# Performance work log

Measured on AMD Instinct MI355X. Metric: run time of the kernel, lower is better.

The kernel has to match this reference:

```python
import jax, jax.numpy as jnp
import numpy as np

B, C, H, Wd = 4, 2048, 64, 64
HID = 256


def setup_inputs() -> dict:
    key = jax.random.key(0)
    k1, k2, k3, k4 = jax.random.split(key, 4)
    return {
        "query_features": jax.random.normal(k1, (B, C, H, Wd), dtype=jnp.float32),
        "prompt_features": jax.random.normal(k2, (B, C, H, Wd), dtype=jnp.float32),
        "W": jax.random.normal(k3, (HID, C), dtype=jnp.float32) * (1.0 / np.sqrt(C)),
        "b": jax.random.normal(k4, (HID,), dtype=jnp.float32) * 0.02,
    }


def reference(query_features, prompt_features, W, b):
    # 1x1 conv == channel projection
    Q = jnp.einsum('bchw,oc->bohw', query_features, W) + b[None, :, None, None]
    K = jnp.einsum('bchw,oc->bohw', prompt_features, W) + b[None, :, None, None]
    Bq, Cf, Hq, Wq = prompt_features.shape
    V = prompt_features.reshape(Bq, Cf, Hq * Wq)              # b c p
    # full pairwise score tensor: bijkl -> b i j (k l)
    attn = jnp.einsum('bcij,bckl->bijkl', Q, K).reshape(Bq, Hq, Wq, Hq * Wq)
    attn = jax.nn.softmax(attn, axis=3)
    aligned = jnp.einsum('bijp,bcp->bcij', attn, V)           # b c h w
    return aligned
```

## Files before the change

### kernel.cpp

```cpp
#include <hip/hip_runtime.h>
#include <math.h>


#define BATCH 4
#define CH    2048
#define PP    4096
#define DD    256

typedef __bf16    bf16x8 __attribute__((ext_vector_type(8)));
typedef _Float16  f16x8  __attribute__((ext_vector_type(8)));
typedef _Float16  f16x4  __attribute__((ext_vector_type(4)));
typedef float     f32x4  __attribute__((ext_vector_type(4)));

__device__ __forceinline__ unsigned short f2bf(float f) {
  unsigned int u = __float_as_uint(f);
  unsigned int r = u + 0x7fffu + ((u >> 16) & 1u);
  return (unsigned short)(r >> 16);
}

#define GLL(src, dst) \
  __builtin_amdgcn_global_load_lds( \
      (const __attribute__((address_space(1))) unsigned int*)(uintptr_t)(src), \
      (__attribute__((address_space(3))) unsigned int*)(uintptr_t)(dst), 16, 0, 0)

__global__ __launch_bounds__(256) void prep_w(
    const float* __restrict__ W, _Float16* __restrict__ Wf) {
  int i = blockIdx.x * 256 + threadIdx.x;
  float4 v = ((const float4*)W)[i];
  f16x4 h = {(_Float16)v.x, (_Float16)v.y, (_Float16)v.z, (_Float16)v.w};
  ((f16x4*)Wf)[i] = h;
}

__global__ __launch_bounds__(256) void tsplit8(
    const float* __restrict__ Xq, const float* __restrict__ Xp,
    _Float16* __restrict__ Xt8) {
  const int z = blockIdx.z;
  const float* __restrict__ X =
      ((z & 1) ? Xp : Xq) + (size_t)(z >> 1) * CH * PP;
  _Float16* __restrict__ Xt = Xt8 + (size_t)z * CH * PP;

  __shared__ float Ls[64 * 65];
  const int tid = threadIdx.x;
  const int pBase = blockIdx.x * 64, cBase = blockIdx.y * 64;
#pragma unroll
  for (int i = 0; i < 4; ++i) {
    int e = tid + i * 256;
    int c = e >> 4, p4 = e & 15;
    float4 v = *(const float4*)&X[(size_t)(cBase + c) * PP + pBase + p4 * 4];
    Ls[c * 65 + p4 * 4 + 0] = v.x; Ls[c * 65 + p4 * 4 + 1] = v.y;
    Ls[c * 65 + p4 * 4 + 2] = v.z; Ls[c * 65 + p4 * 4 + 3] = v.w;
  }
  __syncthreads();
#pragma unroll
  for (int j = 0; j < 4; ++j) {
    int p = (tid >> 4) + j * 16;
    int c4 = (tid & 15) * 4;
    f16x4 h = {(_Float16)Ls[(c4 + 0) * 65 + p], (_Float16)Ls[(c4 + 1) * 65 + p],
               (_Float16)Ls[(c4 + 2) * 65 + p], (_Float16)Ls[(c4 + 3) * 65 + p]};
    *(f16x4*)&Xt[(size_t)(pBase + p) * CH + cBase + c4] = h;
  }
}

__global__ __launch_bounds__(256) void proj8(
    const _Float16* __restrict__ Xt8, const _Float16* __restrict__ Wf,
    const float* __restrict__ bias,
    unsigned short* __restrict__ Qh, unsigned short* __restrict__ Ql,
    unsigned short* __restrict__ Kh, unsigned short* __restrict__ Kl) {
  const int z = blockIdx.z;
  const _Float16* __restrict__ Xt = Xt8 + (size_t)z * CH * PP;
  unsigned short* __restrict__ Yh =
      ((z & 1) ? Kh : Qh) + (size_t)(z >> 1) * PP * DD;
  unsigned short* __restrict__ Yl =
      ((z & 1) ? Kl : Ql) + (size_t)(z >> 1) * PP * DD;

  const int pBase = blockIdx.x * 64;
  const int oBase = blockIdx.y * 64;
  const int tid  = threadIdx.x;
  const int wave = tid >> 6;
  const int lane = tid & 63;
  const int wm = wave & 1, wn = wave >> 1;
  const int row16 = lane & 15, quad = lane >> 4, koff = quad * 8;

  __shared__ __align__(16) _Float16 As0[64 * 32], As1[64 * 32];
  __shared__ __align__(16) _Float16 Bs0[64 * 32], Bs1[64 * 32];

  const int sRow = lane >> 2;
  const int sKc  = (lane & 3) * 8;

  f32x4 acc[2][2];
#pragma unroll
  for (int i = 0; i < 2; ++i)
#pragma unroll
    for (int j = 0; j < 2; ++j) acc[i][j] = (f32x4){0.f, 0.f, 0.f, 0.f};

  for (int c0 = 0; c0 < CH; c0 += 64) {
    const int row = wave * 16 + sRow;
    GLL(&Xt[(size_t)(pBase + row) * CH + c0 + sKc],      &As0[(wave * 16) * 32]);
    GLL(&Xt[(size_t)(pBase + row) * CH + c0 + 32 + sKc], &As1[(wave * 16) * 32]);
    GLL(&Wf[(size_t)(oBase + row) * CH + c0 + sKc],      &Bs0[(wave * 16) * 32]);
    GLL(&Wf[(size_t)(oBase + row) * CH + c0 + 32 + sKc], &Bs1[(wave * 16) * 32]);
    __syncthreads();
#pragma unroll
    for (int s = 0; s < 2; ++s) {
      const _Float16* Ap = s ? As1 : As0;
      const _Float16* Bp = s ? Bs1 : Bs0;
      f16x8 af[2], bf[2];
#pragma unroll
      for (int i = 0; i < 2; ++i)
        af[i] = *(const f16x8*)&Ap[(wm * 32 + i * 16 + row16) * 32 + koff];
#pragma unroll
      for (int j = 0; j < 2; ++j)
        bf[j] = *(const f16x8*)&Bp[(wn * 32 + j * 16 + row16) * 32 + koff];
#pragma unroll
      for (int i = 0; i < 2; ++i)
#pragma unroll
        for (int j = 0; j < 2; ++j)
          acc[i][j] = __builtin_amdgcn_mfma_f32_16x16x32_f16(
              af[i], bf[j], acc[i][j], 0, 0, 0);
    }
    __syncthreads();
  }

#pragma unroll
  for (int i = 0; i < 2; ++i)
#pragma unroll
    for (int j = 0; j < 2; ++j) {
      const int ocol = oBase + wn * 32 + j * 16 + row16;
      const float bv = bias[ocol];
#pragma unroll
      for (int r = 0; r < 4; ++r) {
        const int prow = pBase + wm * 32 + i * 16 + quad * 4 + r;
        float y = acc[i][j][r] + bv;
        unsigned short h = f2bf(y);
        float hf = __uint_as_float((unsigned int)h << 16);
        unsigned short l = f2bf(y - hf);
        Yh[(size_t)prow * DD + ocol] = h;
        Yl[(size_t)prow * DD + ocol] = l;
      }
    }
}

__global__ __launch_bounds__(256) void scores8(
    const unsigned short* __restrict__ Qh_, const unsigned short* __restrict__ Ql_,
    const unsigned short* __restrict__ Kh_, const unsigned short* __restrict__ Kl_,
    float* __restrict__ S_) {
  const size_t z = blockIdx.z;
  const unsigned short* __restrict__ Qh = Qh_ + z * (size_t)PP * DD;
  const unsigned short* __restrict__ Ql = Ql_ + z * (size_t)PP * DD;
  const unsigned short* __restrict__ Kh = Kh_ + z * (size_t)PP * DD;
  const unsigned short* __restrict__ Kl = Kl_ + z * (size_t)PP * DD;
  float* __restrict__ S = S_ + z * (size_t)PP * PP;

  const int kBase = blockIdx.x * 128;
  const int pBase = blockIdx.y * 128;
  const int tid  = threadIdx.x;
  const int wave = tid >> 6;
  const int lane = tid & 63;
  const int wm = wave & 1, wn = wave >> 1;
  const int row16 = lane & 15, quad = lane >> 4, koff = quad * 8;

  __shared__ __align__(16) unsigned short Ah[128 * 32], Al[128 * 32];
  __shared__ __align__(16) unsigned short Bh[128 * 32], Bl[128 * 32];

  const int sRow = lane >> 2;
  const int sKc  = (lane & 3) * 8;

  f32x4 acc[4][4];
#pragma unroll
  for (int i = 0; i < 4; ++i)
#pragma unroll
    for (int j = 0; j < 4; ++j) acc[i][j] = (f32x4){0.f, 0.f, 0.f, 0.f};

  for (int d0 = 0; d0 < DD; d0 += 32) {
#pragma unroll
    for (int t = 0; t < 2; ++t) {
      const int rg = wave * 32 + t * 16;
      const int row = rg + sRow;
      GLL(&Qh[(size_t)(pBase + row) * DD + d0 + sKc], &Ah[rg * 32]);
      GLL(&Ql[(size_t)(pBase + row) * DD + d0 + sKc], &Al[rg * 32]);
      GLL(&Kh[(size_t)(kBase + row) * DD + d0 + sKc], &Bh[rg * 32]);
      GLL(&Kl[(size_t)(kBase + row) * DD + d0 + sKc], &Bl[rg * 32]);
    }
    __syncthreads();
    bf16x8 ah[4], al[4], bh[4], bl[4];
#pragma unroll
    for (int i = 0; i < 4; ++i) {
      ah[i] = *(const bf16x8*)&Ah[(wm * 64 + i * 16 + row16) * 32 + koff];
      al[i] = *(const bf16x8*)&Al[(wm * 64 + i * 16 + row16) * 32 + koff];
    }
#pragma unroll
    for (int j = 0; j < 4; ++j) {
      bh[j] = *(const bf16x8*)&Bh[(wn * 64 + j * 16 + row16) * 32 + koff];
      bl[j] = *(const bf16x8*)&Bl[(wn * 64 + j * 16 + row16) * 32 + koff];
    }
#pragma unroll
    for (int i = 0; i < 4; ++i)
#pragma unroll
      for (int j = 0; j < 4; ++j) {
        acc[i][j] = __builtin_amdgcn_mfma_f32_16x16x32_bf16(ah[i], bh[j], acc[i][j], 0, 0, 0);
        acc[i][j] = __builtin_amdgcn_mfma_f32_16x16x32_bf16(ah[i], bl[j], acc[i][j], 0, 0, 0);
        acc[i][j] = __builtin_amdgcn_mfma_f32_16x16x32_bf16(al[i], bh[j], acc[i][j], 0, 0, 0);
      }
    __syncthreads();
  }

#pragma unroll
  for (int i = 0; i < 4; ++i)
#pragma unroll
    for (int j = 0; j < 4; ++j) {
      const int kcol = kBase + wn * 64 + j * 16 + row16;
#pragma unroll
      for (int r = 0; r < 4; ++r) {
        const int prow = pBase + wm * 64 + i * 16 + quad * 4 + r;
        S[(size_t)prow * PP + kcol] = acc[i][j][r];
      }
    }
}

__global__ __launch_bounds__(256) void softmax8(float* __restrict__ S_) {
  float* __restrict__ Sb = S_ + (size_t)blockIdx.y * PP * PP;
  unsigned short* __restrict__ Ab = (unsigned short*)Sb;
  const size_t p = blockIdx.x;
  float* row = Sb + p * PP;
  const int tid = threadIdx.x;
  float4 v[4];
#pragma unroll
  for (int i = 0; i < 4; ++i)
    v[i] = *(const float4*)&row[(i * 256 + tid) * 4];
  float m = -1e30f;
#pragma unroll
  for (int i = 0; i < 4; ++i)
    m = fmaxf(m, fmaxf(fmaxf(v[i].x, v[i].y), fmaxf(v[i].z, v[i].w)));
#pragma unroll
  for (int off = 32; off > 0; off >>= 1)
    m = fmaxf(m, __shfl_xor(m, off));
  __shared__ float red[4];
  const int lane = tid & 63, wv = tid >> 6;
  if (lane == 0) red[wv] = m;
  __syncthreads();
  m = fmaxf(fmaxf(red[0], red[1]), fmaxf(red[2], red[3]));
  __syncthreads();
  float s = 0.f;
#pragma unroll
  for (int i = 0; i < 4; ++i) {
    v[i].x = __expf(v[i].x - m);
    v[i].y = __expf(v[i].y - m);
    v[i].z = __expf(v[i].z - m);
    v[i].w = __expf(v[i].w - m);
    s += v[i].x + v[i].y + v[i].z + v[i].w;
  }
#pragma unroll
  for (int off = 32; off > 0; off >>= 1)
    s += __shfl_xor(s, off);
  if (lane == 0) red[wv] = s;
  __syncthreads();
  s = red[0] + red[1] + red[2] + red[3];
  const float inv = 1.f / s;
  unsigned short* orow = Ab + p * 8192;
#pragma unroll
  for (int i = 0; i < 4; ++i) {
    ushort4 o;
    o.x = f2bf(v[i].x * inv); o.y = f2bf(v[i].y * inv);
    o.z = f2bf(v[i].z * inv); o.w = f2bf(v[i].w * inv);
    *(ushort4*)&orow[(i * 256 + tid) * 4] = o;
  }
}

__global__ __launch_bounds__(256) void cvt_bf16(
    const float* __restrict__ X, unsigned short* __restrict__ Y, int n4) {
  int i = blockIdx.x * blockDim.x + threadIdx.x;
  if (i < n4) {
    float4 v = ((const float4*)X)[i];
    ushort4 o;
    o.x = f2bf(v.x); o.y = f2bf(v.y); o.z = f2bf(v.z); o.w = f2bf(v.w);
    ((ushort4*)Y)[i] = o;
  }
}


#define AOFF(d, h) ((d) * 32768 + (h) * 16384)
#define BOFF(d, h) (65536 + (d) * 32768 + (h) * 16384)

#define PH_READ_A(d, mh) do {                                                  \
  _Pragma("unroll")                                                            \
  for (int m_ = 0; m_ < 4; ++m_) {                                             \
    const int ro_ = AOFF(d, wm) + ((mh) * 64 + m_ * 16 + row16) * 128;         \
    aR[m_][0] = *(const bf16x8*)(Lds + ro_ + cx0);                             \
    aR[m_][1] = *(const bf16x8*)(Lds + ro_ + cx1);                             \
  } } while (0)

#define PH_READ_B(d, nh, breg) do {                                            \
  _Pragma("unroll")                                                            \
  for (int n_ = 0; n_ < 2; ++n_) {                                             \
    const int ro_ = BOFF(d, wnh) + (wnl * 64 + (nh) * 32 + n_ * 16 + row16) * 128; \
    breg[n_][0] = *(const bf16x8*)(Lds + ro_ + cx0);                           \
    breg[n_][1] = *(const bf16x8*)(Lds + ro_ + cx1);                           \
  } } while (0)

#define PH_MFMA(mh, nh, breg) do {                                             \
  __builtin_amdgcn_s_setprio(1);                                               \
  _Pragma("unroll")                                                            \
  for (int m_ = 0; m_ < 4; ++m_)                                               \
  _Pragma("unroll")                                                            \
  for (int n_ = 0; n_ < 2; ++n_) {                                             \
    f32x4 a_ = acc[(mh) * 4 + m_][(nh) * 2 + n_];                              \
    a_ = __builtin_amdgcn_mfma_f32_16x16x32_bf16(aR[m_][0], breg[n_][0], a_, 0, 0, 0); \
    a_ = __builtin_amdgcn_mfma_f32_16x16x32_bf16(aR[m_][1], breg[n_][1], a_, 0, 0, 0); \
    acc[(mh) * 4 + m_][(nh) * 2 + n_] = a_;                                    \
  }                                                                            \
  __builtin_amdgcn_s_setprio(0); } while (0)

#define BAR_MID() do {                                                         \
  __builtin_amdgcn_sched_barrier(0);                                           \
  __builtin_amdgcn_s_barrier();                                                \
  asm volatile("s_waitcnt lgkmcnt(0)" ::: "memory");                           \
  __builtin_amdgcn_sched_barrier(0); } while (0)

#define BAR_END() __builtin_amdgcn_s_barrier()

__global__ __launch_bounds__(512, 2) void out8(
    const unsigned short* __restrict__ V_,
    const unsigned short* __restrict__ A_,
    float* __restrict__ O_) {
  const size_t z = blockIdx.z;
  const unsigned short* __restrict__ Vb = V_ + z * (size_t)CH * PP;
  const unsigned short* __restrict__ Ab = A_ + z * (size_t)PP * 8192;
  float* __restrict__ Ob = O_ + z * (size_t)CH * PP;

  const int pBase = blockIdx.x * 256;
  const int cBase = blockIdx.y * 256;
  const int tid = threadIdx.x;
  const int wave = tid >> 6, lane = tid & 63;
  const int wm = wave >> 2;
  const int wn = wave & 3;
  const int wnh = wn >> 1, wnl = wn & 1;
  const int row16 = lane & 15, quad = lane >> 4;

  __shared__ __align__(16) char Lds[131072];

  const int swz = (row16 & 7) << 4;
  const int cx0 = ((quad) << 4) ^ swz;
  const int cx1 = ((4 + quad) << 4) ^ swz;

  const int stRow0 = (wave * 2 + 0) * 8 + (lane >> 3);
  const int stRow1 = (wave * 2 + 1) * 8 + (lane >> 3);
  const int stCol  = (((lane & 7) ^ (lane >> 3)) << 4);
  char* ldsSt0 = Lds + (wave * 2 + 0) * 1024;
  char* ldsSt1 = Lds + (wave * 2 + 1) * 1024;

  const size_t VLDG = (size_t)PP * 2;
  const size_t ALDG = (size_t)8192 * 2;

  auto STG = [&](int ldsOff, const void* gbase, size_t ldgB, int rowBase, int gkB) {
    const char* g0 = (const char*)gbase + (size_t)(rowBase + stRow0) * ldgB + gkB + stCol;
    const char* g1 = (const char*)gbase + (size_t)(rowBase + stRow1) * ldgB + gkB + stCol;
    GLL(g0, ldsSt0 + ldsOff);
    GLL(g1, ldsSt1 + ldsOff);
  };

  f32x4 acc[8][4];
#pragma unroll
  for (int i = 0; i < 8; ++i)
#pragma unroll
    for (int j = 0; j < 4; ++j) acc[i][j] = (f32x4){0.f, 0.f, 0.f, 0.f};

  bf16x8 aR[4][2], bLo[2][2], bHi[2][2];

  STG(BOFF(0, 0), Ab, ALDG, pBase + 0,   0);
  STG(BOFF(0, 1), Ab, ALDG, pBase + 128, 0);
  STG(AOFF(0, 0), Vb, VLDG, cBase + 0,   0);
  STG(AOFF(0, 1), Vb, VLDG, cBase + 128, 0);
  STG(BOFF(1, 0), Ab, ALDG, pBase + 0,   128);
  STG(BOFF(1, 1), Ab, ALDG, pBase + 128, 128);
  asm volatile("s_waitcnt vmcnt(4)" ::: "memory");
  __builtin_amdgcn_s_barrier();

#pragma unroll 1
  for (int i = 0; i < 31; ++i) {
    const int t = 2 * i;
    const int gk1 = (t + 1) * 128, gk2 = (t + 2) * 128, gk3 = (t + 3) * 128;
    PH_READ_A(0, 0); PH_READ_B(0, 0, bLo);
    STG(AOFF(1, 0), Vb, VLDG, cBase + 0, gk1);
    BAR_MID(); PH_MFMA(0, 0, bLo); BAR_END();
    PH_READ_B(0, 1, bHi);
    STG(AOFF(1, 1), Vb, VLDG, cBase + 128, gk1);
    BAR_MID(); PH_MFMA(0, 1, bHi); BAR_END();
    PH_READ_A(0, 1);
    STG(BOFF(0, 0), Ab, ALDG, pBase + 0, gk2);
    BAR_MID(); PH_MFMA(1, 0, bLo); BAR_END();
    STG(BOFF(0, 1), Ab, ALDG, pBase + 128, gk2);
    BAR_MID(); PH_MFMA(1, 1, bHi);
    asm volatile("s_waitcnt vmcnt(4)" ::: "memory");
    BAR_END();
    PH_READ_A(1, 0); PH_READ_B(1, 0, bLo);
    STG(AOFF(0, 0), Vb, VLDG, cBase + 0, gk2);
    BAR_MID(); PH_MFMA(0, 0, bLo); BAR_END();
    PH_READ_B(1, 1, bHi);
    STG(AOFF(0, 1), Vb, VLDG, cBase + 128, gk2);
    BAR_MID(); PH_MFMA(0, 1, bHi); BAR_END();
    PH_READ_A(1, 1);
    STG(BOFF(1, 0), Ab, ALDG, pBase + 0, gk3);
    BAR_MID(); PH_MFMA(1, 0, bLo); BAR_END();
    STG(BOFF(1, 1), Ab, ALDG, pBase + 128, gk3);
    BAR_MID(); PH_MFMA(1, 1, bHi);
    asm volatile("s_waitcnt vmcnt(4)" ::: "memory");
    BAR_END();
  }

  {
    const int gk1 = 63 * 128;
    PH_READ_A(0, 0); PH_READ_B(0, 0, bLo);
    STG(AOFF(1, 0), Vb, VLDG, cBase + 0, gk1);
    BAR_MID(); PH_MFMA(0, 0, bLo); BAR_END();
    PH_READ_B(0, 1, bHi);
    STG(AOFF(1, 1), Vb, VLDG, cBase + 128, gk1);
    BAR_MID(); PH_MFMA(0, 1, bHi); BAR_END();
    PH_READ_A(0, 1);
    BAR_MID(); PH_MFMA(1, 0, bLo); BAR_END();
    BAR_MID(); PH_MFMA(1, 1, bHi);
    asm volatile("s_waitcnt vmcnt(0)" ::: "memory");
    BAR_END();
    PH_READ_A(1, 0); PH_READ_B(1, 0, bLo);
    BAR_MID(); PH_MFMA(0, 0, bLo); BAR_END();
    PH_READ_B(1, 1, bHi);
    BAR_MID(); PH_MFMA(0, 1, bHi); BAR_END();
    PH_READ_A(1, 1);
    BAR_MID(); PH_MFMA(1, 0, bLo); BAR_END();
    BAR_MID(); PH_MFMA(1, 1, bHi);
  }

#pragma unroll
  for (int mi = 0; mi < 8; ++mi)
#pragma unroll
    for (int nj = 0; nj < 4; ++nj) {
      const int col = pBase + wn * 64 + nj * 16 + row16;
      float* orow = Ob + (size_t)(cBase + wm * 128 + mi * 16 + quad * 4) * PP + col;
#pragma unroll
      for (int r = 0; r < 4; ++r)
        orow[(size_t)r * PP] = acc[mi][nj][r];
    }
}

extern "C" void kernel_launch(void* const* d_in, const int* in_sizes, int n_in,
                              void* d_out, int out_size, void* d_ws, size_t ws_size,
                              hipStream_t stream) {
  const float* Xq   = (const float*)d_in[0];
  const float* Xp   = (const float*)d_in[1];
  const float* Wg   = (const float*)d_in[2];
  const float* bias = (const float*)d_in[3];
  float* out = (float*)d_out;

  char* w = (char*)d_ws;
  const size_t MB = 1024 * 1024;
  const size_t CHPP = (size_t)CH * PP;

  if (ws_size >= 481 * MB) {
    _Float16* Wf       = (_Float16*)w;
    _Float16* Xt8      = (_Float16*)(w + 1 * MB);
    unsigned short* Qh = (unsigned short*)(w + 129 * MB);
    unsigned short* Ql = (unsigned short*)(w + 137 * MB);
    unsigned short* Kh = (unsigned short*)(w + 145 * MB);
    unsigned short* Kl = (unsigned short*)(w + 153 * MB);
    unsigned short* Vbf = (unsigned short*)(w + 161 * MB);
    float* S           = (float*)(w + 225 * MB);

    prep_w<<<512, 256, 0, stream>>>(Wg, Wf);
    tsplit8<<<dim3(PP / 64, CH / 64, 2 * BATCH), 256, 0, stream>>>(Xq, Xp, Xt8);
    proj8<<<dim3(PP / 64, DD / 64, 2 * BATCH), 256, 0, stream>>>(
        Xt8, Wf, bias, Qh, Ql, Kh, Kl);
    scores8<<<dim3(PP / 128, PP / 128, BATCH), 256, 0, stream>>>(Qh, Ql, Kh, Kl, S);
    softmax8<<<dim3(PP, BATCH), 256, 0, stream>>>(S);
    const int n4t = BATCH * CH * PP / 4;
    cvt_bf16<<<n4t / 256, 256, 0, stream>>>(Xp, Vbf, n4t);
    out8<<<dim3(PP / 256, CH / 256, BATCH), 512, 0, stream>>>(
        Vbf, (unsigned short*)S, out);
  } else {
    _Float16* Xt      = (_Float16*)w;
    unsigned short* Vbf = (unsigned short*)w;
    _Float16* Wf      = (_Float16*)(w + 16 * MB);
    unsigned short* Qh = (unsigned short*)(w + 17 * MB);
    unsigned short* Ql = (unsigned short*)(w + 19 * MB);
    unsigned short* Kh = (unsigned short*)(w + 21 * MB);
    unsigned short* Kl = (unsigned short*)(w + 23 * MB);
    float* S          = (float*)(w + 25 * MB);

    prep_w<<<512, 256, 0, stream>>>(Wg, Wf);
    const int n4 = CH * PP / 4;
    for (int b = 0; b < BATCH; ++b) {
      const float* Xqb = Xq + (size_t)b * CHPP;
      const float* Xpb = Xp + (size_t)b * CHPP;
      tsplit8<<<dim3(PP / 64, CH / 64, 1), 256, 0, stream>>>(Xqb, Xqb, Xt);
      proj8<<<dim3(PP / 64, DD / 64, 1), 256, 0, stream>>>(
          Xt, Wf, bias, Qh, Ql, Qh, Ql);
      tsplit8<<<dim3(PP / 64, CH / 64, 1), 256, 0, stream>>>(Xpb, Xpb, Xt);
      proj8<<<dim3(PP / 64, DD / 64, 1), 256, 0, stream>>>(
          Xt, Wf, bias, Kh, Kl, Kh, Kl);
      scores8<<<dim3(PP / 128, PP / 128, 1), 256, 0, stream>>>(Qh, Ql, Kh, Kl, S);
      softmax8<<<dim3(PP, 1), 256, 0, stream>>>(S);
      cvt_bf16<<<n4 / 256, 256, 0, stream>>>(Xpb, Vbf, n4);
      out8<<<dim3(PP / 256, CH / 256, 1), 512, 0, stream>>>(
          Vbf, (unsigned short*)S, out + (size_t)b * CHPP);
    }
  }
}
```

Before: 874.9 us.

## Pipeline scores GEMM with 256x256 tiles and fuse V bf16 conversion

```diff
diff --git a/kernel.cpp b/kernel.cpp
--- a/kernel.cpp
+++ b/kernel.cpp
@@ -33,11 +33,13 @@
 
 __global__ __launch_bounds__(256) void tsplit8(
     const float* __restrict__ Xq, const float* __restrict__ Xp,
-    _Float16* __restrict__ Xt8) {
+    _Float16* __restrict__ Xt8, unsigned short* __restrict__ Vb8, int doV) {
   const int z = blockIdx.z;
   const float* __restrict__ X =
       ((z & 1) ? Xp : Xq) + (size_t)(z >> 1) * CH * PP;
   _Float16* __restrict__ Xt = Xt8 + (size_t)z * CH * PP;
+  unsigned short* __restrict__ Vb = Vb8 + (size_t)(z >> 1) * CH * PP;
+  const int emitV = doV & z;
 
   __shared__ float Ls[64 * 65];
   const int tid = threadIdx.x;
@@ -49,6 +51,11 @@
     float4 v = *(const float4*)&X[(size_t)(cBase + c) * PP + pBase + p4 * 4];
     Ls[c * 65 + p4 * 4 + 0] = v.x; Ls[c * 65 + p4 * 4 + 1] = v.y;
     Ls[c * 65 + p4 * 4 + 2] = v.z; Ls[c * 65 + p4 * 4 + 3] = v.w;
+    if (emitV) {
+      ushort4 o;
+      o.x = f2bf(v.x); o.y = f2bf(v.y); o.z = f2bf(v.z); o.w = f2bf(v.w);
+      *(ushort4*)&Vb[(size_t)(cBase + c) * PP + pBase + p4 * 4] = o;
+    }
   }
   __syncthreads();
 #pragma unroll
@@ -140,83 +147,6 @@
     }
 }
 
-__global__ __launch_bounds__(256) void scores8(
-    const unsigned short* __restrict__ Qh_, const unsigned short* __restrict__ Ql_,
-    const unsigned short* __restrict__ Kh_, const unsigned short* __restrict__ Kl_,
-    float* __restrict__ S_) {
-  const size_t z = blockIdx.z;
-  const unsigned short* __restrict__ Qh = Qh_ + z * (size_t)PP * DD;
-  const unsigned short* __restrict__ Ql = Ql_ + z * (size_t)PP * DD;
-  const unsigned short* __restrict__ Kh = Kh_ + z * (size_t)PP * DD;
-  const unsigned short* __restrict__ Kl = Kl_ + z * (size_t)PP * DD;
-  float* __restrict__ S = S_ + z * (size_t)PP * PP;
-
-  const int kBase = blockIdx.x * 128;
-  const int pBase = blockIdx.y * 128;
-  const int tid  = threadIdx.x;
-  const int wave = tid >> 6;
-  const int lane = tid & 63;
-  const int wm = wave & 1, wn = wave >> 1;
-  const int row16 = lane & 15, quad = lane >> 4, koff = quad * 8;
-
-  __shared__ __align__(16) unsigned short Ah[128 * 32], Al[128 * 32];
-  __shared__ __align__(16) unsigned short Bh[128 * 32], Bl[128 * 32];
-
-  const int sRow = lane >> 2;
-  const int sKc  = (lane & 3) * 8;
-
-  f32x4 acc[4][4];
-#pragma unroll
-  for (int i = 0; i < 4; ++i)
-#pragma unroll
-    for (int j = 0; j < 4; ++j) acc[i][j] = (f32x4){0.f, 0.f, 0.f, 0.f};
-
-  for (int d0 = 0; d0 < DD; d0 += 32) {
-#pragma unroll
-    for (int t = 0; t < 2; ++t) {
-      const int rg = wave * 32 + t * 16;
-      const int row = rg + sRow;
-      GLL(&Qh[(size_t)(pBase + row) * DD + d0 + sKc], &Ah[rg * 32]);
-      GLL(&Ql[(size_t)(pBase + row) * DD + d0 + sKc], &Al[rg * 32]);
-      GLL(&Kh[(size_t)(kBase + row) * DD + d0 + sKc], &Bh[rg * 32]);
-      GLL(&Kl[(size_t)(kBase + row) * DD + d0 + sKc], &Bl[rg * 32]);
-    }
-    __syncthreads();
-    bf16x8 ah[4], al[4], bh[4], bl[4];
-#pragma unroll
-    for (int i = 0; i < 4; ++i) {
-      ah[i] = *(const bf16x8*)&Ah[(wm * 64 + i * 16 + row16) * 32 + koff];
-      al[i] = *(const bf16x8*)&Al[(wm * 64 + i * 16 + row16) * 32 + koff];
-    }
-#pragma unroll
-    for (int j = 0; j < 4; ++j) {
-      bh[j] = *(const bf16x8*)&Bh[(wn * 64 + j * 16 + row16) * 32 + koff];
-      bl[j] = *(const bf16x8*)&Bl[(wn * 64 + j * 16 + row16) * 32 + koff];
-    }
-#pragma unroll
-    for (int i = 0; i < 4; ++i)
-#pragma unroll
-      for (int j = 0; j < 4; ++j) {
-        acc[i][j] = __builtin_amdgcn_mfma_f32_16x16x32_bf16(ah[i], bh[j], acc[i][j], 0, 0, 0);
-        acc[i][j] = __builtin_amdgcn_mfma_f32_16x16x32_bf16(ah[i], bl[j], acc[i][j], 0, 0, 0);
-        acc[i][j] = __builtin_amdgcn_mfma_f32_16x16x32_bf16(al[i], bh[j], acc[i][j], 0, 0, 0);
-      }
-    __syncthreads();
-  }
-
-#pragma unroll
-  for (int i = 0; i < 4; ++i)
-#pragma unroll
-    for (int j = 0; j < 4; ++j) {
-      const int kcol = kBase + wn * 64 + j * 16 + row16;
-#pragma unroll
-      for (int r = 0; r < 4; ++r) {
-        const int prow = pBase + wm * 64 + i * 16 + quad * 4 + r;
-        S[(size_t)prow * PP + kcol] = acc[i][j][r];
-      }
-    }
-}
-
 __global__ __launch_bounds__(256) void softmax8(float* __restrict__ S_) {
   float* __restrict__ Sb = S_ + (size_t)blockIdx.y * PP * PP;
   unsigned short* __restrict__ Ab = (unsigned short*)Sb;
@@ -306,6 +236,20 @@
     f32x4 a_ = acc[(mh) * 4 + m_][(nh) * 2 + n_];                              \
     a_ = __builtin_amdgcn_mfma_f32_16x16x32_bf16(aR[m_][0], breg[n_][0], a_, 0, 0, 0); \
     a_ = __builtin_amdgcn_mfma_f32_16x16x32_bf16(aR[m_][1], breg[n_][1], a_, 0, 0, 0); \
+    acc[(mh) * 4 + m_][(nh) * 2 + n_] = a_;                                    \
+  }                                                                            \
+  __builtin_amdgcn_s_setprio(0); } while (0)
+
+#define PH_MFMA3(mh, nh, breg) do {                                            \
+  __builtin_amdgcn_s_setprio(1);                                               \
+  _Pragma("unroll")                                                            \
+  for (int m_ = 0; m_ < 4; ++m_)                                               \
+  _Pragma("unroll")                                                            \
+  for (int n_ = 0; n_ < 2; ++n_) {                                             \
+    f32x4 a_ = acc[(mh) * 4 + m_][(nh) * 2 + n_];                              \
+    a_ = __builtin_amdgcn_mfma_f32_16x16x32_bf16(aR[m_][0], breg[n_][0], a_, 0, 0, 0); \
+    a_ = __builtin_amdgcn_mfma_f32_16x16x32_bf16(aR[m_][0], breg[n_][1], a_, 0, 0, 0); \
+    a_ = __builtin_amdgcn_mfma_f32_16x16x32_bf16(aR[m_][1], breg[n_][0], a_, 0, 0, 0); \
     acc[(mh) * 4 + m_][(nh) * 2 + n_] = a_;                                    \
   }                                                                            \
   __builtin_amdgcn_s_setprio(0); } while (0)
@@ -441,6 +385,131 @@
     }
 }
 
+__global__ __launch_bounds__(512, 2) void scr8(
+    const unsigned short* __restrict__ Qh_, const unsigned short* __restrict__ Ql_,
+    const unsigned short* __restrict__ Kh_, const unsigned short* __restrict__ Kl_,
+    float* __restrict__ S_) {
+  const size_t z = blockIdx.z;
+  const unsigned short* __restrict__ Qh = Qh_ + z * (size_t)PP * DD;
+  const unsigned short* __restrict__ Ql = Ql_ + z * (size_t)PP * DD;
+  const unsigned short* __restrict__ Kh = Kh_ + z * (size_t)PP * DD;
+  const unsigned short* __restrict__ Kl = Kl_ + z * (size_t)PP * DD;
+  float* __restrict__ S = S_ + z * (size_t)PP * PP;
+
+  const int kBase = blockIdx.x * 256;
+  const int pBase = blockIdx.y * 256;
+  const int tid = threadIdx.x;
+  const int wave = tid >> 6, lane = tid & 63;
+  const int wm = wave >> 2;
+  const int wn = wave & 3;
+  const int wnh = wn >> 1, wnl = wn & 1;
+  const int row16 = lane & 15, quad = lane >> 4;
+
+  __shared__ __align__(16) char Lds[131072];
+
+  const int swz = (row16 & 7) << 4;
+  const int cx0 = ((quad) << 4) ^ swz;
+  const int cx1 = ((4 + quad) << 4) ^ swz;
+
+  const int stRow0 = (wave * 2 + 0) * 8 + (lane >> 3);
+  const int stRow1 = (wave * 2 + 1) * 8 + (lane >> 3);
+  const int cc   = (lane & 7) ^ (lane >> 3);
+  const int ccB  = (cc & 3) * 16;
+  const char* tQ = (const char*)((cc >> 2) ? Ql : Qh);
+  const char* tK = (const char*)((cc >> 2) ? Kl : Kh);
+  char* ldsSt0 = Lds + (wave * 2 + 0) * 1024;
+  char* ldsSt1 = Lds + (wave * 2 + 1) * 1024;
+
+  auto STG = [&](int ldsOff, const char* tbase, int rowBase, int tkB) {
+    const char* g0 = tbase + (size_t)(rowBase + stRow0) * 512 + tkB + ccB;
+    const char* g1 = tbase + (size_t)(rowBase + stRow1) * 512 + tkB + ccB;
+    GLL(g0, ldsSt0 + ldsOff);
+    GLL(g1, ldsSt1 + ldsOff);
+  };
+
+  f32x4 acc[8][4];
+#pragma unroll
+  for (int i = 0; i < 8; ++i)
+#pragma unroll
+    for (int j = 0; j < 4; ++j) acc[i][j] = (f32x4){0.f, 0.f, 0.f, 0.f};
+
+  bf16x8 aR[4][2], bLo[2][2], bHi[2][2];
+
+  STG(BOFF(0, 0), tK, kBase + 0,   0);
+  STG(BOFF(0, 1), tK, kBase + 128, 0);
+  STG(AOFF(0, 0), tQ, pBase + 0,   0);
+  STG(AOFF(0, 1), tQ, pBase + 128, 0);
+  STG(BOFF(1, 0), tK, kBase + 0,   64);
+  STG(BOFF(1, 1), tK, kBase + 128, 64);
+  asm volatile("s_waitcnt vmcnt(4)" ::: "memory");
+  __builtin_amdgcn_s_barrier();
+
+#pragma unroll 1
+  for (int i = 0; i < 3; ++i) {
+    const int t = 2 * i;
+    const int gk1 = (t + 1) * 64, gk2 = (t + 2) * 64, gk3 = (t + 3) * 64;
+    PH_READ_A(0, 0); PH_READ_B(0, 0, bLo);
+    STG(AOFF(1, 0), tQ, pBase + 0, gk1);
+    BAR_MID(); PH_MFMA3(0, 0, bLo); BAR_END();
+    PH_READ_B(0, 1, bHi);
+    STG(AOFF(1, 1), tQ, pBase + 128, gk1);
+    BAR_MID(); PH_MFMA3(0, 1, bHi); BAR_END();
+    PH_READ_A(0, 1);
+    STG(BOFF(0, 0), tK, kBase + 0, gk2);
+    BAR_MID(); PH_MFMA3(1, 0, bLo); BAR_END();
+    STG(BOFF(0, 1), tK, kBase + 128, gk2);
+    BAR_MID(); PH_MFMA3(1, 1, bHi);
+    asm volatile("s_waitcnt vmcnt(4)" ::: "memory");
+    BAR_END();
+    PH_READ_A(1, 0); PH_READ_B(1, 0, bLo);
+    STG(AOFF(0, 0), tQ, pBase + 0, gk2);
+    BAR_MID(); PH_MFMA3(0, 0, bLo); BAR_END();
+    PH_READ_B(1, 1, bHi);
+    STG(AOFF(0, 1), tQ, pBase + 128, gk2);
+    BAR_MID(); PH_MFMA3(0, 1, bHi); BAR_END();
+    PH_READ_A(1, 1);
+    STG(BOFF(1, 0), tK, kBase + 0, gk3);
+    BAR_MID(); PH_MFMA3(1, 0, bLo); BAR_END();
+    STG(BOFF(1, 1), tK, kBase + 128, gk3);
+    BAR_MID(); PH_MFMA3(1, 1, bHi);
+    asm volatile("s_waitcnt vmcnt(4)" ::: "memory");
+    BAR_END();
+  }
+
+  {
+    const int gk1 = 7 * 64;
+    PH_READ_A(0, 0); PH_READ_B(0, 0, bLo);
+    STG(AOFF(1, 0), tQ, pBase + 0, gk1);
+    BAR_MID(); PH_MFMA3(0, 0, bLo); BAR_END();
+    PH_READ_B(0, 1, bHi);
+    STG(AOFF(1, 1), tQ, pBase + 128, gk1);
+    BAR_MID(); PH_MFMA3(0, 1, bHi); BAR_END();
+    PH_READ_A(0, 1);
+    BAR_MID(); PH_MFMA3(1, 0, bLo); BAR_END();
+    BAR_MID(); PH_MFMA3(1, 1, bHi);
+    asm volatile("s_waitcnt vmcnt(0)" ::: "memory");
+    BAR_END();
+    PH_READ_A(1, 0); PH_READ_B(1, 0, bLo);
+    BAR_MID(); PH_MFMA3(0, 0, bLo); BAR_END();
+    PH_READ_B(1, 1, bHi);
+    BAR_MID(); PH_MFMA3(0, 1, bHi); BAR_END();
+    PH_READ_A(1, 1);
+    BAR_MID(); PH_MFMA3(1, 0, bLo); BAR_END();
+    BAR_MID(); PH_MFMA3(1, 1, bHi);
+  }
+
+#pragma unroll
+  for (int mi = 0; mi < 8; ++mi)
+#pragma unroll
+    for (int nj = 0; nj < 4; ++nj) {
+      const int kcol = kBase + wn * 64 + nj * 16 + row16;
+      float* orow = S + (size_t)(pBase + wm * 128 + mi * 16 + quad * 4) * PP + kcol;
+#pragma unroll
+      for (int r = 0; r < 4; ++r)
+        orow[(size_t)r * PP] = acc[mi][nj][r];
+    }
+}
+
 extern "C" void kernel_launch(void* const* d_in, const int* in_sizes, int n_in,
                               void* d_out, int out_size, void* d_ws, size_t ws_size,
                               hipStream_t stream) {
@@ -465,13 +534,12 @@
     float* S           = (float*)(w + 225 * MB);
 
     prep_w<<<512, 256, 0, stream>>>(Wg, Wf);
-    tsplit8<<<dim3(PP / 64, CH / 64, 2 * BATCH), 256, 0, stream>>>(Xq, Xp, Xt8);
+    tsplit8<<<dim3(PP / 64, CH / 64, 2 * BATCH), 256, 0, stream>>>(
+        Xq, Xp, Xt8, Vbf, 1);
     proj8<<<dim3(PP / 64, DD / 64, 2 * BATCH), 256, 0, stream>>>(
         Xt8, Wf, bias, Qh, Ql, Kh, Kl);
-    scores8<<<dim3(PP / 128, PP / 128, BATCH), 256, 0, stream>>>(Qh, Ql, Kh, Kl, S);
+    scr8<<<dim3(PP / 256, PP / 256, BATCH), 512, 0, stream>>>(Qh, Ql, Kh, Kl, S);
     softmax8<<<dim3(PP, BATCH), 256, 0, stream>>>(S);
-    const int n4t = BATCH * CH * PP / 4;
-    cvt_bf16<<<n4t / 256, 256, 0, stream>>>(Xp, Vbf, n4t);
     out8<<<dim3(PP / 256, CH / 256, BATCH), 512, 0, stream>>>(
         Vbf, (unsigned short*)S, out);
   } else {
@@ -489,13 +557,15 @@
     for (int b = 0; b < BATCH; ++b) {
       const float* Xqb = Xq + (size_t)b * CHPP;
       const float* Xpb = Xp + (size_t)b * CHPP;
-      tsplit8<<<dim3(PP / 64, CH / 64, 1), 256, 0, stream>>>(Xqb, Xqb, Xt);
+      tsplit8<<<dim3(PP / 64, CH / 64, 1), 256, 0, stream>>>(
+          Xqb, Xqb, Xt, Vbf, 0);
       proj8<<<dim3(PP / 64, DD / 64, 1), 256, 0, stream>>>(
           Xt, Wf, bias, Qh, Ql, Qh, Ql);
-      tsplit8<<<dim3(PP / 64, CH / 64, 1), 256, 0, stream>>>(Xpb, Xpb, Xt);
+      tsplit8<<<dim3(PP / 64, CH / 64, 1), 256, 0, stream>>>(
+          Xpb, Xpb, Xt, Vbf, 0);
       proj8<<<dim3(PP / 64, DD / 64, 1), 256, 0, stream>>>(
           Xt, Wf, bias, Kh, Kl, Kh, Kl);
-      scores8<<<dim3(PP / 128, PP / 128, 1), 256, 0, stream>>>(Qh, Ql, Kh, Kl, S);
+      scr8<<<dim3(PP / 256, PP / 256, 1), 512, 0, stream>>>(Qh, Ql, Kh, Kl, S);
       softmax8<<<dim3(PP, 1), 256, 0, stream>>>(S);
       cvt_bf16<<<n4 / 256, 256, 0, stream>>>(Xpb, Vbf, n4);
       out8<<<dim3(PP / 256, CH / 256, 1), 512, 0, stream>>>(
```

Result: faster. 828.5 us (-5.3%).
